# Kernel tuning notes

Measured on AMD Instinct MI355X. Metric: run time of the kernel, lower is better.

## Reference

```python
import jax, jax.numpy as jnp
import numpy as np

B, N, IN, H, I, A, NA, NH = 4096, 8, 256, 256, 64, 64, 32, 256
VAR_FLOOR = 0.002
BN_EPS = 1e-5


def _lin(x, w, b):
    # torch Linear: x @ w.T + b, w: [out, in]
    return x @ w.T + b


def _bn_train(x, g, b):
    # BatchNorm1d in training mode: batch stats, biased variance
    mu = jnp.mean(x, axis=0)
    var = jnp.var(x, axis=0)
    return (x - mu) * jax.lax.rsqrt(var + BN_EPS) * g + b


def _intent_net(h_la, w1, b1, g, bbn, w2, b2):
    z = _lin(h_la, w1, b1)
    z = _bn_train(z, g, bbn)
    z = jax.nn.leaky_relu(z, 0.01)
    return _lin(z, w2, b2)


def setup_inputs() -> dict:
    key = jax.random.key(0)
    ks = jax.random.split(key, 30)
    s = 0.05
    d = {
        "inputs": jax.random.normal(ks[0], (B * N, IN), jnp.float32),
        "last_actions": jax.random.normal(ks[1], (B, N, NA), jnp.float32),
        "hidden_state": jax.random.normal(ks[2], (B * N, H), jnp.float32),
        "eps": jax.random.normal(ks[3], (B * N, I), jnp.float32),
        # fc1
        "fc1_w": jax.random.normal(ks[4], (H, IN), jnp.float32) * s,
        "fc1_b": jnp.zeros((H,), jnp.float32),
        # GRUCell (r,z,n gate order, torch layout)
        "gru_w_ih": jax.random.normal(ks[5], (3 * H, H), jnp.float32) * s,
        "gru_w_hh": jax.random.normal(ks[6], (3 * H, H), jnp.float32) * s,
        "gru_b_ih": jnp.zeros((3 * H,), jnp.float32),
        "gru_b_hh": jnp.zeros((3 * H,), jnp.float32),
        # intent_net: Linear(H+NA, NH) -> BN -> LeakyReLU -> Linear(NH, 2*I)
        "in1_w": jax.random.normal(ks[7], (NH, H + NA), jnp.float32) * s,
        "in1_b": jnp.zeros((NH,), jnp.float32),
        "bn_g": jnp.ones((NH,), jnp.float32),
        "bn_b": jnp.zeros((NH,), jnp.float32),
        "in2_w": jax.random.normal(ks[8], (2 * I, NH), jnp.float32) * s,
        "in2_b": jnp.zeros((2 * I,), jnp.float32),
        # attention projections
        "wq_w": jax.random.normal(ks[9], (A, I), jnp.float32) * s,
        "wq_b": jnp.zeros((A,), jnp.float32),
        "wk_w": jax.random.normal(ks[10], (A, I), jnp.float32) * s,
        "wk_b": jnp.zeros((A,), jnp.float32),
        "wv_w": jax.random.normal(ks[11], (A, I + H), jnp.float32) * s,
        "wv_b": jnp.zeros((A,), jnp.float32),
        # fc2
        "fc2_w": jax.random.normal(ks[12], (NA, H + A), jnp.float32) * s,
        "fc2_b": jnp.zeros((NA,), jnp.float32),
        "bs": B,
        "t": 1,
    }
    return d


def reference(inputs, last_actions, hidden_state, eps,
              fc1_w, fc1_b, gru_w_ih, gru_w_hh, gru_b_ih, gru_b_hh,
              in1_w, in1_b, bn_g, bn_b, in2_w, in2_b,
              wq_w, wq_b, wk_w, wk_b, wv_w, wv_b, fc2_w, fc2_b,
              bs, t):
    n = N
    x = jax.nn.relu(_lin(inputs, fc1_w, fc1_b))  # [bs*n, H]
    h_in = hidden_state.reshape(-1, H)
    # torch GRUCell
    gi = x @ gru_w_ih.T + gru_b_ih
    gh = h_in @ gru_w_hh.T + gru_b_hh
    i_r, i_z, i_n = jnp.split(gi, 3, axis=-1)
    h_r, h_z, h_n = jnp.split(gh, 3, axis=-1)
    r = jax.nn.sigmoid(i_r + h_r)
    z = jax.nn.sigmoid(i_z + h_z)
    nng = jnp.tanh(i_n + r * h_n)
    h = (1.0 - z) * nng + z * h_in  # [bs*n, H]

    la = last_actions.reshape(bs * n, NA)
    h_la = jnp.concatenate([h, la], axis=-1)
    ip = _intent_net(h_la, in1_w, in1_b, bn_g, bn_b, in2_w, in2_b)  # [bs*n, 2I]
    mean = ip[:, :I]
    std = jnp.maximum(jnp.exp(ip[:, I:]), VAR_FLOOR)
    intent = mean + eps * std  # reparameterized sample, [bs*n, I]

    q = _lin(intent, wq_w, wq_b).reshape(bs, n, A)  # query per agent i
    k = _lin(intent, wk_w, wk_b).reshape(bs, n, A)  # key per agent j
    scale = 1.0 / jnp.sqrt(jnp.float32(A))
    alpha = jnp.einsum('bia,bja->bij', q * scale, k)  # [bs, n, n]
    diag = jnp.eye(n, dtype=bool)
    alpha = jnp.where(diag[None], -1e9, alpha)
    alpha = jax.nn.softmax(alpha, axis=-1)

    v = _lin(jnp.concatenate([intent, h], axis=-1), wv_w, wv_b).reshape(bs, n, A)
    combined = jnp.einsum('bij,bja->bia', alpha, v).reshape(bs * n, A)

    local_Q = _lin(jnp.concatenate([h, combined], axis=-1), fc2_w, fc2_b).reshape(bs, n, NA)
    # final intent_embed: fresh intent_net output (no clamp/exp applied)
    intent_embed = _intent_net(h_la, in1_w, in1_b, bn_g, bn_b, in2_w, in2_b)
    return local_Q, h, intent, intent_embed
```

## Files before the change

### kernel.cpp

```cpp
#include <hip/hip_runtime.h>
#include <hip/hip_bf16.h>

#define BN_ 32768

using bf16 = __hip_bfloat16;
typedef __bf16 v8bf __attribute__((ext_vector_type(8)));
typedef unsigned short v8us __attribute__((ext_vector_type(8)));
typedef float v4f __attribute__((ext_vector_type(4)));

__device__ __forceinline__ float b2f(bf16 x) { return __bfloat162float(x); }
__device__ __forceinline__ bf16 f2b(float x) { return __float2bfloat16(x); }
__device__ __forceinline__ unsigned short f2bu(float x) {
  bf16 h = __float2bfloat16(x);
  return *reinterpret_cast<unsigned short*>(&h);
}
__device__ __forceinline__ float bu2f(unsigned short u) {
  union { unsigned int i; float f; } x;
  x.i = ((unsigned int)u) << 16;
  return x.f;
}
__device__ __forceinline__ void gl_lds16(const void* g, void* l) {
  __builtin_amdgcn_global_load_lds(
      (const __attribute__((address_space(1))) void*)g,
      (__attribute__((address_space(3))) void*)l, 16, 0, 0);
}
__device__ __forceinline__ float fsig(float x) { return 1.f / (1.f + __expf(-x)); }
__device__ __forceinline__ float ftanh(float x) {
  return 1.f - 2.f / (__expf(2.f * x) + 1.f);
}
template <int CF>
__device__ __forceinline__ void cstore(void* C, size_t off, float v) {
  if constexpr (CF) ((float*)C)[off] = v;
  else ((bf16*)C)[off] = f2b(v);
}
__device__ __forceinline__ int xcd_swz() {
  const int nbx = gridDim.x, nby = gridDim.y;
  const int f = blockIdx.y * nbx + blockIdx.x;
  const int nwg = nbx * nby;
  const int q = nwg >> 3, r = nwg & 7;
  const int xcd = f & 7, l = f >> 3;
  if (r == 0) return xcd * q + l;
  return (xcd < r ? xcd * (q + 1) : r * (q + 1) + (xcd - r) * q) + l;
}

template <int TM, int TN, int WR, int WC, int ACT, int A1M, int A2M, int KS, int KSB,
          int CF, int ATF, int STATS, int QKV>
__global__ __launch_bounds__(256) void gemm_bt(
    const void* __restrict__ A1, int lda1, const void* __restrict__ A2, int lda2,
    const bf16* __restrict__ B1, const bf16* __restrict__ B2, int ldb,
    const float* __restrict__ bias, void* C, int ldc, int K,
    const float* __restrict__ tsc, const float* __restrict__ tsh,
    float* __restrict__ PART, const float* __restrict__ pe,
    float* __restrict__ pit, unsigned short* __restrict__ pitb, void* C2) {
  constexpr int BK = 64;
  __shared__ __align__(16) unsigned short As[TM * BK];
  __shared__ __align__(16) unsigned short Bs[TN * BK];
  const int tid = threadIdx.x;
  const int wv = tid >> 6;
  const int lane = tid & 63;
  const int w = xcd_swz();
  const int bm = (w / gridDim.y) * TM;
  const int bn = (w % gridDim.y) * TN;

  constexpr int WM = TM / WR, WN = TN / WC;
  constexpr int FM = WM / 16, FN = WN / 16;
  const int wm0 = (wv % WR) * WM;
  const int wn0 = (wv / WR) * WN;

  v4f acc[FM][FN];
  const v4f vzero = {0.f, 0.f, 0.f, 0.f};
  for (int i = 0; i < FM; ++i)
    for (int j = 0; j < FN; ++j) acc[i][j] = vzero;

  const int lrow = lane >> 3;
  const int lcol = (lane & 7) * 8;
  const int mr = lane & 15;
  const int kq = (lane >> 4) * 8;

  for (int k0 = 0; k0 < K; k0 += BK) {
    {
      const bool useA1 = (KS == 0) || (k0 < KS);
      const void* Ap = useA1 ? A1 : A2;
      const int lda = useA1 ? lda1 : lda2;
      const int ka = useA1 ? k0 : k0 - KS;
      const bool f32 = useA1 ? (A1M == 1) : (A2M == 1);
      if (ATF && useA1) {
        const unsigned short* Ab = (const unsigned short*)Ap;
        const float4 s0 = *(const float4*)(tsc + ka + lcol);
        const float4 s1 = *(const float4*)(tsc + ka + lcol + 4);
        const float4 h0 = *(const float4*)(tsh + ka + lcol);
        const float4 h1 = *(const float4*)(tsh + ka + lcol + 4);
        const float sc[8] = {s0.x, s0.y, s0.z, s0.w, s1.x, s1.y, s1.z, s1.w};
        const float sh[8] = {h0.x, h0.y, h0.z, h0.w, h1.x, h1.y, h1.z, h1.w};
        for (int ch = wv; ch < TM / 8; ch += 4) {
          const unsigned short* s = Ab + (size_t)(bm + ch * 8 + lrow) * lda + ka + lcol;
          v8us zin = *(const v8us*)s;
          v8us d;
#pragma unroll
          for (int u = 0; u < 8; ++u) {
            float v = bu2f(zin[u]) * sc[u] + sh[u];
            d[u] = f2bu(v > 0.f ? v : 0.01f * v);
          }
          *(v8us*)(As + ch * 8 * BK + lane * 8) = d;
        }
      } else if (f32) {
        const float* Af = (const float*)Ap;
        for (int ch = wv; ch < TM / 8; ch += 4) {
          const float* s = Af + (size_t)(bm + ch * 8 + lrow) * lda + ka + lcol;
          float4 x0 = *(const float4*)s;
          float4 x1 = *(const float4*)(s + 4);
          v8us d;
          d[0]=f2bu(x0.x); d[1]=f2bu(x0.y); d[2]=f2bu(x0.z); d[3]=f2bu(x0.w);
          d[4]=f2bu(x1.x); d[5]=f2bu(x1.y); d[6]=f2bu(x1.z); d[7]=f2bu(x1.w);
          *(v8us*)(As + ch * 8 * BK + lane * 8) = d;
        }
      } else {
        const unsigned short* Ab = (const unsigned short*)Ap;
        for (int ch = wv; ch < TM / 8; ch += 4)
          gl_lds16(Ab + (size_t)(bm + ch * 8 + lrow) * lda + ka + lcol,
                   As + ch * 8 * BK);
      }
    }
    {
      const bool useB1 = (KSB == 0) || (k0 < KSB);
      const bf16* Bp = useB1 ? B1 : B2;
      const int kb = useB1 ? k0 : k0 - KSB;
      for (int ch = wv; ch < TN / 8; ch += 4)
        gl_lds16((const unsigned short*)Bp + (size_t)(bn + ch * 8 + lrow) * ldb + kb + lcol,
                 Bs + ch * 8 * BK);
    }
    __syncthreads();
#pragma unroll
    for (int kk = 0; kk < BK; kk += 32) {
      v8bf af[FM], bfr[FN];
#pragma unroll
      for (int i = 0; i < FM; ++i)
        af[i] = *(const v8bf*)(As + (wm0 + i * 16 + mr) * BK + kk + kq);
#pragma unroll
      for (int j = 0; j < FN; ++j)
        bfr[j] = *(const v8bf*)(Bs + (wn0 + j * 16 + mr) * BK + kk + kq);
#pragma unroll
      for (int i = 0; i < FM; ++i)
#pragma unroll
        for (int j = 0; j < FN; ++j)
          acc[i][j] = __builtin_amdgcn_mfma_f32_16x16x32_bf16(af[i], bfr[j],
                                                              acc[i][j], 0, 0, 0);
    }
    __syncthreads();
  }
  const int crow = (lane >> 4) * 4;

  if constexpr (ACT == 5) {
#pragma unroll
    for (int j = 0; j < 4; ++j) {
      const int gcol = bn + j * 16 + mr;
      const float bmn = bias[gcol];
      const float bsd = bias[gcol + 64];
#pragma unroll
      for (int r = 0; r < 4; ++r) {
        const int grow = bm + wm0 + crow + r;
        const float mean = acc[0][j][r] + bmn;
        const float lstd = acc[0][j + 4][r] + bsd;
        ((float*)C)[(size_t)grow * 128 + gcol] = mean;
        ((float*)C)[(size_t)grow * 128 + gcol + 64] = lstd;
        const float sd = fmaxf(__expf(lstd), 0.002f);
        const float iv = mean + pe[(size_t)grow * 64 + gcol] * sd;
        pit[(size_t)grow * 64 + gcol] = iv;
        pitb[(size_t)grow * 512 + gcol] = f2bu(iv);
      }
    }
  } else {
#pragma unroll
    for (int j = 0; j < FN; ++j) {
      const int gcol = bn + wn0 + j * 16 + mr;
      const float bv = bias[gcol];
      float ps = 0.f, pq = 0.f;
#pragma unroll
      for (int i = 0; i < FM; ++i) {
#pragma unroll
        for (int r = 0; r < 4; ++r) {
          const int grow = bm + wm0 + i * 16 + crow + r;
          float v = acc[i][j][r] + bv;
          if (ACT == 1) v = v > 0.f ? v : 0.f;
          if constexpr (QKV) {
            if (gcol < 128) ((bf16*)C)[(size_t)grow * 128 + gcol] = f2b(v);
            else ((bf16*)C2)[(size_t)grow * 64 + (gcol - 128)] = f2b(v);
          } else if constexpr (STATS) {
            const unsigned short d = f2bu(v);
            ((bf16*)C)[(size_t)grow * ldc + gcol] = *(const bf16*)&d;
            const float vr = bu2f(d);
            ps += vr; pq += vr * vr;
          } else {
            cstore<CF>(C, (size_t)grow * ldc + gcol, v);
          }
        }
      }
      if constexpr (STATS) {
        ps += __shfl_xor(ps, 16); ps += __shfl_xor(ps, 32);
        pq += __shfl_xor(pq, 16); pq += __shfl_xor(pq, 32);
        if (lane < 16) {
          const int slot = (gcol << 9) + ((bm >> 7) << 1) + (wv % WR);
          PART[slot] = ps;
          PART[131072 + slot] = pq;
        }
      }
    }
  }
}

__global__ __launch_bounds__(64) void bn_finalize2(
    const float* __restrict__ PART, const float* __restrict__ g,
    const float* __restrict__ b, float* __restrict__ stats) {
  const int col = blockIdx.x;
  const int lane = threadIdx.x;
  const float4* ps = (const float4*)(PART + (col << 9));
  const float4* pq = (const float4*)(PART + 131072 + (col << 9));
  float s = 0.f, q = 0.f;
#pragma unroll
  for (int u = 0; u < 2; ++u) {
    const float4 a = ps[lane * 2 + u];
    const float4 c = pq[lane * 2 + u];
    s += a.x + a.y + a.z + a.w;
    q += c.x + c.y + c.z + c.w;
  }
#pragma unroll
  for (int m = 1; m < 64; m <<= 1) {
    s += __shfl_xor(s, m);
    q += __shfl_xor(q, m);
  }
  if (lane == 0) {
    const float mean = s * (1.f / 32768.f);
    float var = q * (1.f / 32768.f) - mean * mean;
    var = fmaxf(var, 0.f);
    const float sc = g[col] * rsqrtf(var + 1e-5f);
    stats[512 + col] = sc;
    stats[768 + col] = b[col] - mean * sc;
  }
}

__global__ __launch_bounds__(256) void gru_fused(
    const bf16* __restrict__ X, const bf16* __restrict__ HB,
    const bf16* __restrict__ Win, const bf16* __restrict__ Whn,
    const float* __restrict__ FBp, const bf16* G1, unsigned short* HB2,
    float* __restrict__ Hout) {
  __shared__ __align__(16) char smem[49152];
  float* Ein = (float*)smem;
  float* Ehn = Ein + 64 * 68;

  const int tid = threadIdx.x;
  const int wv = tid >> 6;
  const int lane = tid & 63;
  const int w = xcd_swz();
  const int bm = (w / gridDim.y) * 64;
  const int bn = (w % gridDim.y) * 128;
  const int wm0 = (wv & 1) * 32;
  const int wn0 = (wv >> 1) * 64;

  v4f ain[2][4], ahn[2][4];
  const v4f vzero = {0.f, 0.f, 0.f, 0.f};
  for (int i = 0; i < 2; ++i)
    for (int j = 0; j < 4; ++j) { ain[i][j] = vzero; ahn[i][j] = vzero; }

  const int lrow2 = lane >> 2;
  const int lcol2 = (lane & 3) * 8;
  const int mr = lane & 15;
  const int kq = (lane >> 4) * 8;

  auto STAGE = [&](int b, int t) {
    unsigned short* base = (unsigned short*)(smem + b * 24576);
    const int k0 = t * 32;
    {
      const size_t aoff = (size_t)(bm + wv * 16 + lrow2) * 256 + k0 + lcol2;
      gl_lds16((const unsigned short*)X + aoff, base + wv * 512);
      gl_lds16((const unsigned short*)HB + aoff, base + 2048 + wv * 512);
    }
    for (int c = wv; c < 8; c += 4) {
      const size_t boff = (size_t)(bn + c * 16 + lrow2) * 256 + k0 + lcol2;
      gl_lds16((const unsigned short*)Win + boff, base + 4096 + c * 512);
      gl_lds16((const unsigned short*)Whn + boff, base + 8192 + c * 512);
    }
  };

  int cur = 0;
  STAGE(0, 0);
  asm volatile("s_waitcnt vmcnt(0)" ::: "memory");
  __builtin_amdgcn_s_barrier();
  for (int t = 0; t < 8; ++t) {
    if (t < 7) STAGE(cur ^ 1, t + 1);
    {
      const unsigned short* base = (const unsigned short*)(smem + cur * 24576);
      v8bf ax[2], ah[2], bi[4], bh[4];
#pragma unroll
      for (int i = 0; i < 2; ++i) {
        ax[i] = *(const v8bf*)(base + (wm0 + i * 16 + mr) * 32 + kq);
        ah[i] = *(const v8bf*)(base + 2048 + (wm0 + i * 16 + mr) * 32 + kq);
      }
#pragma unroll
      for (int j = 0; j < 4; ++j) {
        bi[j] = *(const v8bf*)(base + 4096 + (wn0 + j * 16 + mr) * 32 + kq);
        bh[j] = *(const v8bf*)(base + 8192 + (wn0 + j * 16 + mr) * 32 + kq);
      }
#pragma unroll
      for (int i = 0; i < 2; ++i)
#pragma unroll
        for (int j = 0; j < 4; ++j) {
          ain[i][j] = __builtin_amdgcn_mfma_f32_16x16x32_bf16(ax[i], bi[j],
                                                              ain[i][j], 0, 0, 0);
          ahn[i][j] = __builtin_amdgcn_mfma_f32_16x16x32_bf16(ah[i], bh[j],
                                                              ahn[i][j], 0, 0, 0);
        }
    }
    asm volatile("s_waitcnt vmcnt(0)" ::: "memory");
    __builtin_amdgcn_s_barrier();
    cur ^= 1;
  }

  const int crow = (lane >> 4) * 4;
  const int myhalf = wn0 >> 6;
  const int c4 = (tid & 15) * 4;
#pragma unroll
  for (int h = 0; h < 2; ++h) {
    ushort4 r4a[4], z4a[4], hp4a[4];
#pragma unroll
    for (int it = 0; it < 4; ++it) {
      const int grow = bm + (tid >> 4) + it * 16;
      const int gcol = bn + h * 64 + c4;
      const unsigned short* g1p = (const unsigned short*)G1 + (size_t)grow * 512 + gcol;
      r4a[it] = *(const ushort4*)g1p;
      z4a[it] = *(const ushort4*)(g1p + 256);
      hp4a[it] = *(const ushort4*)((const unsigned short*)HB + (size_t)grow * 256 + gcol);
    }
    __syncthreads();
    if (myhalf == h) {
#pragma unroll
      for (int i = 0; i < 2; ++i)
#pragma unroll
        for (int j = 0; j < 4; ++j)
#pragma unroll
          for (int r = 0; r < 4; ++r) {
            const int idx = (wm0 + i * 16 + crow + r) * 68 + j * 16 + mr;
            Ein[idx] = ain[i][j][r];
            Ehn[idx] = ahn[i][j][r];
          }
    }
    __syncthreads();
#pragma unroll
    for (int it = 0; it < 4; ++it) {
      const int row = (tid >> 4) + it * 16;
      const int grow = bm + row;
      const int gcol = bn + h * 64 + c4;
      const float4 ei = *(const float4*)(Ein + row * 68 + c4);
      const float4 eh = *(const float4*)(Ehn + row * 68 + c4);
      const float4 bin4 = *(const float4*)(FBp + 768 + gcol);
      const float4 bhn4 = *(const float4*)(FBp + 1024 + gcol);
      const float rv[4] = {bu2f(r4a[it].x), bu2f(r4a[it].y), bu2f(r4a[it].z), bu2f(r4a[it].w)};
      const float zv[4] = {bu2f(z4a[it].x), bu2f(z4a[it].y), bu2f(z4a[it].z), bu2f(z4a[it].w)};
      const float hpv[4] = {bu2f(hp4a[it].x), bu2f(hp4a[it].y), bu2f(hp4a[it].z), bu2f(hp4a[it].w)};
      const float eiv[4] = {ei.x, ei.y, ei.z, ei.w};
      const float ehv[4] = {eh.x, eh.y, eh.z, eh.w};
      const float biv[4] = {bin4.x, bin4.y, bin4.z, bin4.w};
      const float bhv[4] = {bhn4.x, bhn4.y, bhn4.z, bhn4.w};
      float vo[4];
#pragma unroll
      for (int u = 0; u < 4; ++u) {
        float rr = fsig(rv[u]);
        float zz = fsig(zv[u]);
        float nn = ftanh(eiv[u] + biv[u] + rr * (ehv[u] + bhv[u]));
        vo[u] = (1.f - zz) * nn + zz * hpv[u];
      }
      *(float4*)(Hout + (size_t)grow * 256 + gcol) =
          make_float4(vo[0], vo[1], vo[2], vo[3]);
      ushort4 hb2;
      hb2.x = f2bu(vo[0]); hb2.y = f2bu(vo[1]);
      hb2.z = f2bu(vo[2]); hb2.w = f2bu(vo[3]);
      *(ushort4*)(HB2 + (size_t)grow * 512 + gcol) = hb2;
    }
  }
}

__global__ void conv_all(
    const float* fc1_w, const float* w_ih, const float* w_hh, const float* in1_w,
    const float* in2_w, const float* wq_w, const float* wk_w, const float* wv_w,
    const float* fc2_w, const float* fc1_b, const float* b_ih, const float* b_hh,
    const float* in1_b, const float* in2_b, const float* wq_b, const float* wk_b,
    const float* wv_b, const float* fc2_b, const float* bn_g, const float* bn_b,
    bf16* __restrict__ WF, float* __restrict__ FB) {
  int idx = blockIdx.x * 256 + threadIdx.x;
  if (idx < 673792) {
    float v;
    if (idx < 65536) v = fc1_w[idx];
    else if (idx < 262144) v = w_ih[idx - 65536];
    else if (idx < 458752) v = w_hh[idx - 262144];
    else if (idx < 540672) {
      int j = idx - 458752, r = j / 320, c = j % 320;
      v = (c < 288) ? in1_w[r * 288 + c] : 0.f;
    } else if (idx < 573440) v = in2_w[idx - 540672];
    else if (idx < 602112) {
      v = (idx >= 573440 && idx < 581632)
              ? 0.f
              : (idx < 602112 ? 0.f : 0.f);
    } else if (idx < 612352) v = fc2_w[idx - 602112];
    else {
      int j = idx - 612352, r = j / 320, c = j % 320;
      if (r < 128) v = (c < 64) ? (r < 64 ? wq_w[r * 64 + c]
                                          : wk_w[(r - 64) * 64 + c]) : 0.f;
      else v = wv_w[(size_t)(r - 128) * 320 + c];
    }
    WF[idx] = f2b(v);
  } else if (idx < 677376) {
    int j = idx - 673792;
    float v;
    if (j < 256) v = fc1_b[j];
    else if (j < 768) v = b_ih[j - 256] + b_hh[j - 256];
    else if (j < 1024) v = b_ih[512 + j - 768];
    else if (j < 1280) v = b_hh[512 + j - 1024];
    else if (j < 1536) v = in1_b[j - 1280];
    else if (j < 1664) v = in2_b[j - 1536];
    else if (j < 1792) { int c = j - 1664; v = (c < 64) ? wq_b[c] : wk_b[c - 64]; }
    else if (j < 1856) v = wv_b[j - 1792];
    else if (j < 1888) v = fc2_b[j - 1856];
    else if (j < 2144) v = bn_g[j - 1888];
    else if (j < 2400) v = bn_b[j - 2144];
    else v = 0.f;
    FB[j] = v;
  }
}

__global__ void pack_all(const float* __restrict__ h, bf16* __restrict__ hb,
                         const float* __restrict__ x, bf16* __restrict__ xb,
                         const float* __restrict__ la, bf16* __restrict__ lap) {
  const int bid = blockIdx.x;
  if (bid < 8192) {
    const float* s = bid < 4096 ? h : x;
    bf16* d = bid < 4096 ? hb : xb;
    const int i = (bid & 4095) * 256 + threadIdx.x;
    const float4 x0 = ((const float4*)s)[i * 2];
    const float4 x1 = ((const float4*)s)[i * 2 + 1];
    v8us o;
    o[0]=f2bu(x0.x); o[1]=f2bu(x0.y); o[2]=f2bu(x0.z); o[3]=f2bu(x0.w);
    o[4]=f2bu(x1.x); o[5]=f2bu(x1.y); o[6]=f2bu(x1.z); o[7]=f2bu(x1.w);
    ((v8us*)d)[i] = o;
  } else {
    const int i = (bid - 8192) * 256 + threadIdx.x;
    const int row = i >> 3, cg = i & 7;
    v8us o;
    if (cg < 4) {
      const float4 a = *(const float4*)(la + (size_t)row * 32 + cg * 8);
      const float4 b = *(const float4*)(la + (size_t)row * 32 + cg * 8 + 4);
      o[0]=f2bu(a.x); o[1]=f2bu(a.y); o[2]=f2bu(a.z); o[3]=f2bu(a.w);
      o[4]=f2bu(b.x); o[5]=f2bu(b.y); o[6]=f2bu(b.z); o[7]=f2bu(b.w);
    } else {
      for (int u = 0; u < 8; ++u) o[u] = 0;
    }
    ((v8us*)lap)[i] = o;
  }
}

__global__ __launch_bounds__(256) void attn(const bf16* __restrict__ QK,
                                            const bf16* __restrict__ Vv,
                                            bf16* __restrict__ comb) {
  __shared__ float q[4][8][65], k[4][8][65], v[4][8][65];
  __shared__ float al[4][8][8];
  const int wv = threadIdx.x >> 6, t = threadIdx.x & 63;
  const int b = blockIdx.x * 4 + wv;
  const size_t rb = (size_t)b * 8;
  const unsigned short* qkb = (const unsigned short*)QK + rb * 128;
#pragma unroll
  for (int p = 0; p < 2; ++p) {
    const int e = t * 8 + p * 512;
    const int row = e >> 7, col = e & 127;
    v8us d = *(const v8us*)(qkb + row * 128 + col);
    if (col < 64) {
#pragma unroll
      for (int u = 0; u < 8; ++u) q[wv][row][col + u] = bu2f(d[u]);
    } else {
#pragma unroll
      for (int u = 0; u < 8; ++u) k[wv][row][col - 64 + u] = bu2f(d[u]);
    }
  }
  {
    const int e = t * 8;
    const int row = e >> 6, col = e & 63;
    v8us d = *(const v8us*)((const unsigned short*)Vv + rb * 64 + row * 64 + col);
#pragma unroll
    for (int u = 0; u < 8; ++u) v[wv][row][col + u] = bu2f(d[u]);
  }
  __syncthreads();
  const int i = t >> 3, j = t & 7;
  float s = 0.f;
#pragma unroll
  for (int a = 0; a < 64; ++a) s += q[wv][i][a] * k[wv][j][a];
  s *= 0.125f;
  if (i == j) s = -1e9f;
  float m = s;
  m = fmaxf(m, __shfl_xor(m, 1, 8));
  m = fmaxf(m, __shfl_xor(m, 2, 8));
  m = fmaxf(m, __shfl_xor(m, 4, 8));
  float e = __expf(s - m);
  float sum = e;
  sum += __shfl_xor(sum, 1, 8);
  sum += __shfl_xor(sum, 2, 8);
  sum += __shfl_xor(sum, 4, 8);
  al[wv][i][j] = e / sum;
  __syncthreads();
  const int a0 = (t & 7) * 8;
  v8us o8;
#pragma unroll
  for (int u = 0; u < 8; ++u) {
    float o = 0.f;
#pragma unroll
    for (int jj = 0; jj < 8; ++jj) o += al[wv][i][jj] * v[wv][jj][a0 + u];
    o8[u] = f2bu(o);
  }
  *(v8us*)((unsigned short*)comb + (rb + i) * 64 + a0) = o8;
}

extern "C" void kernel_launch(void* const* d_in, const int* in_sizes, int n_in,
                              void* d_out, int out_size, void* d_ws, size_t ws_size,
                              hipStream_t stream) {
  (void)in_sizes; (void)n_in; (void)out_size; (void)ws_size;
  const float* inputs = (const float*)d_in[0];
  const float* last_actions = (const float*)d_in[1];
  const float* hidden = (const float*)d_in[2];
  const float* eps = (const float*)d_in[3];

  float* out = (float*)d_out;
  float* out_lq = out;
  float* out_h = out + 1048576;
  float* out_it = out + 9437184;
  float* out_ie = out + 11534336;

  bf16* HB = (bf16*)(out + 11534336);
  bf16* XB = (bf16*)(out + 1048576);
  bf16* LAP = (bf16*)out_lq;
  float* PART = out + 9437184;

  char* ws = (char*)d_ws;
  bf16* X    = (bf16*)(ws + 0);
  bf16* G1   = (bf16*)(ws + 16777216);
  unsigned short* HB2 = (unsigned short*)(ws + 16777216);
  unsigned short* ITB = (unsigned short*)(ws + 16777216) + 256;
  bf16* Z1   = (bf16*)(ws + 0);
  bf16* QK   = (bf16*)(ws + 0);
  bf16* V    = (bf16*)(ws + 8388608);
  bf16* COMB = (bf16*)(ws + 12582912);
  float* FB  = (float*)(ws + 50331648);
  bf16*  WF  = (bf16*)(ws + 50348032);
  float* stats = FB + 2560;

  conv_all<<<2646, 256, 0, stream>>>(
      (const float*)d_in[4], (const float*)d_in[6], (const float*)d_in[7],
      (const float*)d_in[10], (const float*)d_in[14], (const float*)d_in[16],
      (const float*)d_in[18], (const float*)d_in[20], (const float*)d_in[22],
      (const float*)d_in[5], (const float*)d_in[8], (const float*)d_in[9],
      (const float*)d_in[11], (const float*)d_in[15], (const float*)d_in[17],
      (const float*)d_in[19], (const float*)d_in[21], (const float*)d_in[23],
      (const float*)d_in[12], (const float*)d_in[13], WF, FB);

  pack_all<<<9216, 256, 0, stream>>>(hidden, HB, inputs, XB, last_actions, LAP);

  gemm_bt<64, 128, 2, 2, 1, 0, 0, 0, 0, 0, 0, 0, 0><<<dim3(512, 2), 256, 0, stream>>>(
      XB, 256, nullptr, 0, WF + 0, nullptr, 256, FB + 0, X, 256, 256,
      nullptr, nullptr, nullptr, nullptr, nullptr, nullptr, nullptr);
  gemm_bt<64, 128, 2, 2, 0, 0, 0, 256, 256, 0, 0, 0, 0><<<dim3(512, 4), 256, 0, stream>>>(
      X, 256, HB, 256, WF + 65536, WF + 262144, 256, FB + 256, G1, 512, 512,
      nullptr, nullptr, nullptr, nullptr, nullptr, nullptr, nullptr);
  gru_fused<<<dim3(512, 2), 256, 0, stream>>>(
      X, HB, WF + 65536 + 512 * 256, WF + 262144 + 512 * 256, FB, G1, HB2, out_h);

  gemm_bt<128, 128, 2, 2, 0, 0, 0, 256, 0, 0, 0, 1, 0><<<dim3(256, 2), 256, 0, stream>>>(
      HB2, 512, LAP, 64, WF + 458752, nullptr, 320, FB + 1280, Z1, 256, 320,
      nullptr, nullptr, PART, nullptr, nullptr, nullptr, nullptr);
  bn_finalize2<<<256, 64, 0, stream>>>(PART, FB + 1888, FB + 2144, stats);
  gemm_bt<64, 128, 4, 1, 5, 0, 0, 0, 0, 1, 1, 0, 0><<<dim3(512, 1), 256, 0, stream>>>(
      Z1, 256, nullptr, 0, WF + 540672, nullptr, 256, FB + 1536, out_ie, 128, 256,
      stats + 512, stats + 768, nullptr, eps, out_it, ITB, nullptr);
  gemm_bt<64, 192, 2, 2, 0, 0, 0, 64, 0, 0, 0, 0, 1><<<dim3(512, 1), 256, 0, stream>>>(
      ITB, 512, HB2, 512, WF + 612352, nullptr, 320, FB + 1664, QK, 128, 320,
      nullptr, nullptr, nullptr, nullptr, nullptr, nullptr, V);
  attn<<<1024, 256, 0, stream>>>(QK, V, COMB);
  gemm_bt<64, 32, 4, 1, 0, 0, 0, 256, 0, 1, 0, 0, 0><<<dim3(512, 1), 256, 0, stream>>>(
      HB2, 512, COMB, 64, WF + 602112, nullptr, 320, FB + 1856, out_lq, 32, 320,
      nullptr, nullptr, nullptr, nullptr, nullptr, nullptr, nullptr);
}
```

Measured before the change: 323.8 us.

## Use single-buffered BK=64 tiles in GRU kernel and smaller BN-stats GEMM tiles

The GRU n-gate kernel drops its double-buffered BK=32 pipeline in favour of a single-buffered BK=64 tile: all loads for a tile are issued, then one barrier, then compute. This halves the number of k-iterations and barriers but removes the overlap of loads with MFMA work. Separately, the intent-net first GEMM with BN statistics switches from 128-row to 64-row tiles, doubling the grid. The partial-sum buffer layout and bn_finalize2 are widened to match the doubled number of row partials. PART must now hold twice as many floats, and it is not visible whether its allocation was enlarged.

```diff
diff --git a/kernel.cpp b/kernel.cpp
--- a/kernel.cpp
+++ b/kernel.cpp
@@ -199,9 +199,9 @@
         ps += __shfl_xor(ps, 16); ps += __shfl_xor(ps, 32);
         pq += __shfl_xor(pq, 16); pq += __shfl_xor(pq, 32);
         if (lane < 16) {
-          const int slot = (gcol << 9) + ((bm >> 7) << 1) + (wv % WR);
+          const int slot = (gcol << 10) + ((bm >> 6) << 1) + (wv % WR);
           PART[slot] = ps;
-          PART[131072 + slot] = pq;
+          PART[262144 + slot] = pq;
         }
       }
     }
@@ -213,13 +213,13 @@
     const float* __restrict__ b, float* __restrict__ stats) {
   const int col = blockIdx.x;
   const int lane = threadIdx.x;
-  const float4* ps = (const float4*)(PART + (col << 9));
-  const float4* pq = (const float4*)(PART + 131072 + (col << 9));
+  const float4* ps = (const float4*)(PART + (col << 10));
+  const float4* pq = (const float4*)(PART + 262144 + (col << 10));
   float s = 0.f, q = 0.f;
 #pragma unroll
-  for (int u = 0; u < 2; ++u) {
-    const float4 a = ps[lane * 2 + u];
-    const float4 c = pq[lane * 2 + u];
+  for (int u = 0; u < 4; ++u) {
+    const float4 a = ps[lane * 4 + u];
+    const float4 c = pq[lane * 4 + u];
     s += a.x + a.y + a.z + a.w;
     q += c.x + c.y + c.z + c.w;
   }
@@ -243,7 +243,12 @@
     const bf16* __restrict__ Win, const bf16* __restrict__ Whn,
     const float* __restrict__ FBp, const bf16* G1, unsigned short* HB2,
     float* __restrict__ Hout) {
+  constexpr int BK = 64;
   __shared__ __align__(16) char smem[49152];
+  unsigned short* AsX = (unsigned short*)smem;
+  unsigned short* AsH = AsX + 4096;
+  unsigned short* Bin = AsH + 4096;
+  unsigned short* Bhn = Bin + 8192;
   float* Ein = (float*)smem;
   float* Ehn = Ein + 64 * 68;
 
@@ -261,44 +266,35 @@
   for (int i = 0; i < 2; ++i)
     for (int j = 0; j < 4; ++j) { ain[i][j] = vzero; ahn[i][j] = vzero; }
 
-  const int lrow2 = lane >> 2;
-  const int lcol2 = (lane & 3) * 8;
+  const int lrow = lane >> 3;
+  const int lcol = (lane & 7) * 8;
   const int mr = lane & 15;
   const int kq = (lane >> 4) * 8;
 
-  auto STAGE = [&](int b, int t) {
-    unsigned short* base = (unsigned short*)(smem + b * 24576);
-    const int k0 = t * 32;
-    {
-      const size_t aoff = (size_t)(bm + wv * 16 + lrow2) * 256 + k0 + lcol2;
-      gl_lds16((const unsigned short*)X + aoff, base + wv * 512);
-      gl_lds16((const unsigned short*)HB + aoff, base + 2048 + wv * 512);
-    }
-    for (int c = wv; c < 8; c += 4) {
-      const size_t boff = (size_t)(bn + c * 16 + lrow2) * 256 + k0 + lcol2;
-      gl_lds16((const unsigned short*)Win + boff, base + 4096 + c * 512);
-      gl_lds16((const unsigned short*)Whn + boff, base + 8192 + c * 512);
-    }
-  };
-
-  int cur = 0;
-  STAGE(0, 0);
-  asm volatile("s_waitcnt vmcnt(0)" ::: "memory");
-  __builtin_amdgcn_s_barrier();
-  for (int t = 0; t < 8; ++t) {
-    if (t < 7) STAGE(cur ^ 1, t + 1);
-    {
-      const unsigned short* base = (const unsigned short*)(smem + cur * 24576);
+  for (int k0 = 0; k0 < 256; k0 += BK) {
+    for (int ch = wv; ch < 8; ch += 4) {
+      const size_t aoff = (size_t)(bm + ch * 8 + lrow) * 256 + k0 + lcol;
+      gl_lds16((const unsigned short*)X + aoff, AsX + ch * 8 * BK);
+      gl_lds16((const unsigned short*)HB + aoff, AsH + ch * 8 * BK);
+    }
+    for (int ch = wv; ch < 16; ch += 4) {
+      const size_t boff = (size_t)(bn + ch * 8 + lrow) * 256 + k0 + lcol;
+      gl_lds16((const unsigned short*)Win + boff, Bin + ch * 8 * BK);
+      gl_lds16((const unsigned short*)Whn + boff, Bhn + ch * 8 * BK);
+    }
+    __syncthreads();
+#pragma unroll
+    for (int kk = 0; kk < BK; kk += 32) {
       v8bf ax[2], ah[2], bi[4], bh[4];
 #pragma unroll
       for (int i = 0; i < 2; ++i) {
-        ax[i] = *(const v8bf*)(base + (wm0 + i * 16 + mr) * 32 + kq);
-        ah[i] = *(const v8bf*)(base + 2048 + (wm0 + i * 16 + mr) * 32 + kq);
+        ax[i] = *(const v8bf*)(AsX + (wm0 + i * 16 + mr) * BK + kk + kq);
+        ah[i] = *(const v8bf*)(AsH + (wm0 + i * 16 + mr) * BK + kk + kq);
       }
 #pragma unroll
       for (int j = 0; j < 4; ++j) {
-        bi[j] = *(const v8bf*)(base + 4096 + (wn0 + j * 16 + mr) * 32 + kq);
-        bh[j] = *(const v8bf*)(base + 8192 + (wn0 + j * 16 + mr) * 32 + kq);
+        bi[j] = *(const v8bf*)(Bin + (wn0 + j * 16 + mr) * BK + kk + kq);
+        bh[j] = *(const v8bf*)(Bhn + (wn0 + j * 16 + mr) * BK + kk + kq);
       }
 #pragma unroll
       for (int i = 0; i < 2; ++i)
@@ -310,9 +306,7 @@
                                                               ahn[i][j], 0, 0, 0);
         }
     }
-    asm volatile("s_waitcnt vmcnt(0)" ::: "memory");
-    __builtin_amdgcn_s_barrier();
-    cur ^= 1;
+    __syncthreads();
   }
 
   const int crow = (lane >> 4) * 4;
@@ -396,9 +390,7 @@
       v = (c < 288) ? in1_w[r * 288 + c] : 0.f;
     } else if (idx < 573440) v = in2_w[idx - 540672];
     else if (idx < 602112) {
-      v = (idx >= 573440 && idx < 581632)
-              ? 0.f
-              : (idx < 602112 ? 0.f : 0.f);
+      v = 0.f;
     } else if (idx < 612352) v = fc2_w[idx - 602112];
     else {
       int j = idx - 612352, r = j / 320, c = j % 320;
@@ -568,7 +560,7 @@
   gru_fused<<<dim3(512, 2), 256, 0, stream>>>(
       X, HB, WF + 65536 + 512 * 256, WF + 262144 + 512 * 256, FB, G1, HB2, out_h);
 
-  gemm_bt<128, 128, 2, 2, 0, 0, 0, 256, 0, 0, 0, 1, 0><<<dim3(256, 2), 256, 0, stream>>>(
+  gemm_bt<64, 128, 2, 2, 0, 0, 0, 256, 0, 0, 0, 1, 0><<<dim3(512, 2), 256, 0, stream>>>(
       HB2, 512, LAP, 64, WF + 458752, nullptr, 320, FB + 1280, Z1, 256, 320,
       nullptr, nullptr, PART, nullptr, nullptr, nullptr, nullptr);
   bn_finalize2<<<256, 64, 0, stream>>>(PART, FB + 1888, FB + 2144, stats);
```

Measured after the change: 314.0 us. 3.0% less time.
